# Optimization experiments

Measured on AMD Instinct MI355X. Metric: run time of the kernel, lower is better.

Reference implementation:

```python
import jax, jax.numpy as jnp
import numpy as np

TAU = 0.1
N, D = 8192, 128
NUM_CLASSES = 100


def setup_inputs() -> dict:
    key = jax.random.key(0)
    kx, ky = jax.random.split(key)
    x = jax.random.normal(kx, (N, D), dtype=jnp.float32)
    y = jax.random.randint(ky, (N,), 0, NUM_CLASSES, dtype=jnp.int64)
    return {"x": x, "y": y}


def reference(x, y):
    # cosine similarity matrix: S[i,j] = <x_i, x_j> / (||x_i|| ||x_j||)
    norms = jnp.linalg.norm(x, axis=-1, keepdims=True)  # [N,1]
    xn = x / norms
    sim = jnp.einsum('id,jd->ij', xn, xn)               # [N,N]
    e = jnp.exp(sim / TAU)                              # [N,N]
    same = (y[:, None] == y[None, :])                   # [N,N] bool (includes self, as in original)
    top = jnp.sum(jnp.where(same, e, 0.0), axis=1)      # [N]
    down = jnp.sum(e, axis=1)                           # [N]
    loss = jnp.mean(-jnp.log(top / down))
    return loss
```

## Files before the change

kernel.cpp:

```cpp
#include <hip/hip_runtime.h>
#include <hip/hip_bf16.h>
#include <stdint.h>

#define NROWS 8192
#define DDIM  128
#define NCHUNK 16
#define ROWS_PER_BLOCK 128
#define COLS_PER_BLOCK 512
#define GROUP_COLS 64
#define GROUP_BYTES (GROUP_COLS * DDIM)
#define NGROUPS (COLS_PER_BLOCK / GROUP_COLS)

typedef __attribute__((ext_vector_type(4))) float f32x4;
typedef long f8x8;

__device__ __forceinline__ void load_lds16(const void* g, void* l) {
    __builtin_amdgcn_global_load_lds(
        (const __attribute__((address_space(1))) void*)g,
        (__attribute__((address_space(3))) void*)l, 16, 0, 0);
}

#define SCALE 14.426950408889634f
#define E10   22026.465794806718f

__global__ __launch_bounds__(256) void normalize_kernel(
    const float* __restrict__ x, unsigned short* __restrict__ q16,
    float* __restrict__ dsq)
{
    int wave = threadIdx.x >> 6;
    int lane = threadIdx.x & 63;
    int row  = blockIdx.x * 4 + wave;
    const float2* xr = (const float2*)(x + (size_t)row * DDIM);
    float2 v = xr[lane];
    float ss = v.x * v.x + v.y * v.y;
    #pragma unroll
    for (int off = 1; off < 64; off <<= 1)
        ss += __shfl_xor(ss, off, 64);
    float rn = sqrtf(SCALE / ss);
    int pk = __builtin_amdgcn_cvt_pk_fp8_f32(v.x * rn, v.y * rn, 0, false);
    q16[(size_t)row * 64 + lane] = (unsigned short)(pk & 0xffff);
    float d0 = __builtin_amdgcn_cvt_f32_fp8(pk, 0);
    float d1 = __builtin_amdgcn_cvt_f32_fp8(pk, 1);
    float sq = d0 * d0 + d1 * d1;
    #pragma unroll
    for (int off = 1; off < 64; off <<= 1)
        sq += __shfl_xor(sq, off, 64);
    if (lane == 0) dsq[row] = sq;
}

__global__ __launch_bounds__(256, 4) void sim_kernel(
    const unsigned short* __restrict__ q16, const int* __restrict__ y,
    float* __restrict__ topp, float* __restrict__ downp)
{
    __shared__ char smem[2 * GROUP_BYTES];
    __shared__ int  yl[COLS_PER_BLOCK];

    const int bid  = blockIdx.x;
    const int iblk = bid >> 4;
    const int h    = bid & 15;
    const int tid  = threadIdx.x;
    const int lane = tid & 63;
    const int wave = tid >> 6;
    const int lrow = lane & 15;
    const int lhi  = lane >> 4;

    const char* qb = (const char*)q16;
    const int rbase = iblk * ROWS_PER_BLOCK + wave * 32;
    const int jbase = h * COLS_PER_BLOCK;

    yl[tid]       = y[jbase + tid];
    yl[tid + 256] = y[jbase + tid + 256];

    f8x8 afrag[2][4];
    #pragma unroll
    for (int t = 0; t < 2; ++t)
        #pragma unroll
        for (int ks = 0; ks < 4; ++ks)
            afrag[t][ks] = *(const f8x8*)(qb +
                (size_t)(rbase + t * 16 + lrow) * DDIM + ks * 32 + lhi * 8);

    int yrow[2][4];
    #pragma unroll
    for (int t = 0; t < 2; ++t)
        #pragma unroll
        for (int r = 0; r < 4; ++r)
            yrow[t][r] = y[rbase + t * 16 + lhi * 4 + r];

    float top[2][4]  = {{0.f,0.f,0.f,0.f},{0.f,0.f,0.f,0.f}};
    float down[2][4] = {{0.f,0.f,0.f,0.f},{0.f,0.f,0.f,0.f}};

    auto stage = [&](int buf, int g) {
        const int jstart = jbase + g * GROUP_COLS;
        #pragma unroll
        for (int p = 0; p < 2; ++p) {
            int phys = p * 4096 + tid * 16;
            int col  = phys >> 7;
            int L    = phys ^ ((col & 7) << 4);
            const char* src = qb + (size_t)(jstart + col) * DDIM + (L & 127);
            load_lds16(src, smem + buf * GROUP_BYTES + phys);
        }
    };

    stage(0, 0);
    __syncthreads();

    for (int g = 0; g < NGROUPS; ++g) {
        if (g + 1 < NGROUPS) stage((g + 1) & 1, g + 1);

        const char* lbuf = smem + (g & 1) * GROUP_BYTES;

        #pragma unroll
        for (int jt = 0; jt < GROUP_COLS / 16; ++jt) {
            const int cg = jt * 16 + lrow;
            const int ycol = yl[g * GROUP_COLS + cg];
            f8x8 bfrag[4];
            #pragma unroll
            for (int ks = 0; ks < 4; ++ks) {
                int off = cg * DDIM + ((ks * 32 + lhi * 8) ^ ((cg & 7) << 4));
                bfrag[ks] = *(const f8x8*)(lbuf + off);
            }
            #pragma unroll
            for (int t = 0; t < 2; ++t) {
                f32x4 acc = {0.f, 0.f, 0.f, 0.f};
                #pragma unroll
                for (int ks = 0; ks < 4; ++ks)
                    acc = __builtin_amdgcn_mfma_f32_16x16x32_fp8_fp8(
                        afrag[t][ks], bfrag[ks], acc, 0, 0, 0);
                #pragma unroll
                for (int r = 0; r < 4; ++r) {
                    float e = __builtin_amdgcn_exp2f(acc[r]);
                    down[t][r] += e;
                    top[t][r]  += (yrow[t][r] == ycol) ? e : 0.0f;
                }
            }
        }
        __syncthreads();
    }

    #pragma unroll
    for (int m = 1; m < 16; m <<= 1) {
        #pragma unroll
        for (int t = 0; t < 2; ++t)
            #pragma unroll
            for (int r = 0; r < 4; ++r) {
                top[t][r]  += __shfl_xor(top[t][r],  m, 64);
                down[t][r] += __shfl_xor(down[t][r], m, 64);
            }
    }

    if (lrow == 0) {
        #pragma unroll
        for (int t = 0; t < 2; ++t)
            #pragma unroll
            for (int r = 0; r < 4; ++r) {
                int row = rbase + t * 16 + lhi * 4 + r;
                topp [h * NROWS + row] = top[t][r];
                downp[h * NROWS + row] = down[t][r];
            }
    }
}

__global__ __launch_bounds__(64) void loss_partial_kernel(
    const float* __restrict__ topp, const float* __restrict__ downp,
    const float* __restrict__ dsq, float* __restrict__ partial)
{
    const int lane = threadIdx.x;
    const int r = blockIdx.x * 64 + lane;
    float t = 0.f, d = 0.f;
    #pragma unroll
    for (int hh = 0; hh < NCHUNK; ++hh) {
        t += topp [hh * NROWS + r];
        d += downp[hh * NROWS + r];
    }
    float e2d = __builtin_amdgcn_exp2f(dsq[r]);
    t = t - e2d + E10;
    d = d - e2d + E10;
    float s = __logf(d) - __logf(t);
    #pragma unroll
    for (int off = 1; off < 64; off <<= 1)
        s += __shfl_xor(s, off, 64);
    if (lane == 0) partial[blockIdx.x] = s;
}

__global__ __launch_bounds__(64) void loss_final_kernel(
    const float* __restrict__ partial, float* __restrict__ out)
{
    const int lane = threadIdx.x;
    float s = partial[lane] + partial[lane + 64];
    #pragma unroll
    for (int off = 1; off < 64; off <<= 1)
        s += __shfl_xor(s, off, 64);
    if (lane == 0) out[0] = s / (float)NROWS;
}

extern "C" void kernel_launch(void* const* d_in, const int* in_sizes, int n_in,
                              void* d_out, int out_size, void* d_ws, size_t ws_size,
                              hipStream_t stream)
{
    const float* x = (const float*)d_in[0];
    const int*   y = (const int*)d_in[1];
    float* out = (float*)d_out;

    char* ws = (char*)d_ws;
    unsigned short* q16 = (unsigned short*)ws;
    float* topp  = (float*)(ws + (size_t)NROWS * DDIM);
    float* downp = topp + NCHUNK * NROWS;
    float* dsq     = downp + NCHUNK * NROWS;
    float* partial = dsq + NROWS;

    normalize_kernel<<<NROWS / 4, 256, 0, stream>>>(x, q16, dsq);
    sim_kernel<<<64 * NCHUNK, 256, 0, stream>>>(q16, y, topp, downp);
    loss_partial_kernel<<<NROWS / 64, 64, 0, stream>>>(topp, downp, dsq, partial);
    loss_final_kernel<<<1, 64, 0, stream>>>(partial, out);
}
```

Measured before the change: 36.30 us.

## Retile sim kernel to 256x256 tiles with single-shot LDS panel load

The similarity kernel now gives each block 256 rows by 256 columns: each wave keeps 64 rows of A fragments in registers, and the whole 32KB column panel is loaded into LDS once up front. This replaces the 128x512 tiling and its double-buffered 64-column staging. Each B fragment read from LDS is now reused across four row tiles instead of two, and the per-group barriers go away. The cost is more registers per thread, which may reduce occupancy. There is also no overlap between the panel load and compute, and the number of column chunks the later reduction must sum doubles.

```diff
diff --git a/kernel.cpp b/kernel.cpp
--- a/kernel.cpp
+++ b/kernel.cpp
@@ -4,12 +4,10 @@
 
 #define NROWS 8192
 #define DDIM  128
-#define NCHUNK 16
-#define ROWS_PER_BLOCK 128
-#define COLS_PER_BLOCK 512
-#define GROUP_COLS 64
-#define GROUP_BYTES (GROUP_COLS * DDIM)
-#define NGROUPS (COLS_PER_BLOCK / GROUP_COLS)
+#define NCHUNK 32
+#define ROWS_PER_BLOCK 256
+#define COLS_PER_BLOCK 256
+#define PANEL_BYTES (COLS_PER_BLOCK * DDIM)
 
 typedef __attribute__((ext_vector_type(4))) float f32x4;
 typedef long f8x8;
@@ -52,12 +50,12 @@
     const unsigned short* __restrict__ q16, const int* __restrict__ y,
     float* __restrict__ topp, float* __restrict__ downp)
 {
-    __shared__ char smem[2 * GROUP_BYTES];
+    __shared__ char smem[PANEL_BYTES];
     __shared__ int  yl[COLS_PER_BLOCK];
 
     const int bid  = blockIdx.x;
-    const int iblk = bid >> 4;
-    const int h    = bid & 15;
+    const int iblk = bid >> 5;
+    const int h    = bid & 31;
     const int tid  = threadIdx.x;
     const int lane = tid & 63;
     const int wave = tid >> 6;
@@ -65,82 +63,70 @@
     const int lhi  = lane >> 4;
 
     const char* qb = (const char*)q16;
-    const int rbase = iblk * ROWS_PER_BLOCK + wave * 32;
+    const int rbase = iblk * ROWS_PER_BLOCK + wave * 64;
     const int jbase = h * COLS_PER_BLOCK;
 
-    yl[tid]       = y[jbase + tid];
-    yl[tid + 256] = y[jbase + tid + 256];
-
-    f8x8 afrag[2][4];
-    #pragma unroll
-    for (int t = 0; t < 2; ++t)
+    yl[tid] = y[jbase + tid];
+
+    #pragma unroll
+    for (int p = 0; p < 8; ++p) {
+        int phys = p * 4096 + tid * 16;
+        int col  = phys >> 7;
+        int L    = phys ^ ((col & 7) << 4);
+        const char* src = qb + (size_t)(jbase + col) * DDIM + (L & 127);
+        load_lds16(src, smem + phys);
+    }
+
+    f8x8 afrag[4][4];
+    #pragma unroll
+    for (int t = 0; t < 4; ++t)
         #pragma unroll
         for (int ks = 0; ks < 4; ++ks)
             afrag[t][ks] = *(const f8x8*)(qb +
                 (size_t)(rbase + t * 16 + lrow) * DDIM + ks * 32 + lhi * 8);
 
-    int yrow[2][4];
-    #pragma unroll
-    for (int t = 0; t < 2; ++t)
+    int yrow[4][4];
+    #pragma unroll
+    for (int t = 0; t < 4; ++t)
         #pragma unroll
         for (int r = 0; r < 4; ++r)
             yrow[t][r] = y[rbase + t * 16 + lhi * 4 + r];
 
-    float top[2][4]  = {{0.f,0.f,0.f,0.f},{0.f,0.f,0.f,0.f}};
-    float down[2][4] = {{0.f,0.f,0.f,0.f},{0.f,0.f,0.f,0.f}};
-
-    auto stage = [&](int buf, int g) {
-        const int jstart = jbase + g * GROUP_COLS;
-        #pragma unroll
-        for (int p = 0; p < 2; ++p) {
-            int phys = p * 4096 + tid * 16;
-            int col  = phys >> 7;
-            int L    = phys ^ ((col & 7) << 4);
-            const char* src = qb + (size_t)(jstart + col) * DDIM + (L & 127);
-            load_lds16(src, smem + buf * GROUP_BYTES + phys);
+    float top[4][4]  = {};
+    float down[4][4] = {};
+
+    __syncthreads();
+
+    #pragma unroll 2
+    for (int jt = 0; jt < COLS_PER_BLOCK / 16; ++jt) {
+        const int cg = jt * 16 + lrow;
+        const int ycol = yl[cg];
+        f8x8 bfrag[4];
+        #pragma unroll
+        for (int ks = 0; ks < 4; ++ks) {
+            int off = cg * DDIM + ((ks * 32 + lhi * 8) ^ ((cg & 7) << 4));
+            bfrag[ks] = *(const f8x8*)(smem + off);
         }
-    };
-
-    stage(0, 0);
-    __syncthreads();
-
-    for (int g = 0; g < NGROUPS; ++g) {
-        if (g + 1 < NGROUPS) stage((g + 1) & 1, g + 1);
-
-        const char* lbuf = smem + (g & 1) * GROUP_BYTES;
-
-        #pragma unroll
-        for (int jt = 0; jt < GROUP_COLS / 16; ++jt) {
-            const int cg = jt * 16 + lrow;
-            const int ycol = yl[g * GROUP_COLS + cg];
-            f8x8 bfrag[4];
-            #pragma unroll
-            for (int ks = 0; ks < 4; ++ks) {
-                int off = cg * DDIM + ((ks * 32 + lhi * 8) ^ ((cg & 7) << 4));
-                bfrag[ks] = *(const f8x8*)(lbuf + off);
-            }
-            #pragma unroll
-            for (int t = 0; t < 2; ++t) {
-                f32x4 acc = {0.f, 0.f, 0.f, 0.f};
-                #pragma unroll
-                for (int ks = 0; ks < 4; ++ks)
-                    acc = __builtin_amdgcn_mfma_f32_16x16x32_fp8_fp8(
-                        afrag[t][ks], bfrag[ks], acc, 0, 0, 0);
-                #pragma unroll
-                for (int r = 0; r < 4; ++r) {
-                    float e = __builtin_amdgcn_exp2f(acc[r]);
-                    down[t][r] += e;
-                    top[t][r]  += (yrow[t][r] == ycol) ? e : 0.0f;
-                }
+        #pragma unroll
+        for (int t = 0; t < 4; ++t) {
+            f32x4 acc = {0.f, 0.f, 0.f, 0.f};
+            #pragma unroll
+            for (int ks = 0; ks < 4; ++ks)
+                acc = __builtin_amdgcn_mfma_f32_16x16x32_fp8_fp8(
+                    afrag[t][ks], bfrag[ks], acc, 0, 0, 0);
+            #pragma unroll
+            for (int r = 0; r < 4; ++r) {
+                float e = __builtin_amdgcn_exp2f(acc[r]);
+                down[t][r] += e;
+                top[t][r]  += (yrow[t][r] == ycol) ? e : 0.0f;
             }
         }
-        __syncthreads();
     }
 
     #pragma unroll
     for (int m = 1; m < 16; m <<= 1) {
         #pragma unroll
-        for (int t = 0; t < 2; ++t)
+        for (int t = 0; t < 4; ++t)
             #pragma unroll
             for (int r = 0; r < 4; ++r) {
                 top[t][r]  += __shfl_xor(top[t][r],  m, 64);
@@ -150,7 +136,7 @@
 
     if (lrow == 0) {
         #pragma unroll
-        for (int t = 0; t < 2; ++t)
+        for (int t = 0; t < 4; ++t)
             #pragma unroll
             for (int r = 0; r < 4; ++r) {
                 int row = rbase + t * 16 + lhi * 4 + r;
@@ -209,7 +195,7 @@
     float* partial = dsq + NROWS;
 
     normalize_kernel<<<NROWS / 4, 256, 0, stream>>>(x, q16, dsq);
-    sim_kernel<<<64 * NCHUNK, 256, 0, stream>>>(q16, y, topp, downp);
+    sim_kernel<<<(NROWS / ROWS_PER_BLOCK) * NCHUNK, 256, 0, stream>>>(q16, y, topp, downp);
     loss_partial_kernel<<<NROWS / 64, 64, 0, stream>>>(topp, downp, dsq, partial);
     loss_final_kernel<<<1, 64, 0, stream>>>(partial, out);
 }
```

Measured after the change: 55.76 us. 1.54x slower.

## Exploit similarity symmetry by computing only upper-triangular tile pairs

Applied to the files above, without the earlier changes.

The similarity kernel now launches one block per unordered 128x128 tile pair (i<=j) and recovers the pair indices from a triangular index. Each off-diagonal tile adds its exp values to both row sums and column sums. Column partials are reduced across lanes and waves through LDS and written to the transposed slot, which roughly halves the MFMA and exp work. In exchange it adds column reduction, extra syncs and LDS, and the final reduction reads 64 partial chunks instead of 16, adding memory traffic.

```diff
diff --git a/kernel.cpp b/kernel.cpp
--- a/kernel.cpp
+++ b/kernel.cpp
@@ -4,12 +4,11 @@
 
 #define NROWS 8192
 #define DDIM  128
-#define NCHUNK 16
-#define ROWS_PER_BLOCK 128
-#define COLS_PER_BLOCK 512
-#define GROUP_COLS 64
-#define GROUP_BYTES (GROUP_COLS * DDIM)
-#define NGROUPS (COLS_PER_BLOCK / GROUP_COLS)
+#define NBLK  64
+#define NPAIR (NBLK * (NBLK + 1) / 2)
+#define BI 128
+#define BJ 128
+#define PANEL_BYTES (BJ * DDIM)
 
 typedef __attribute__((ext_vector_type(4))) float f32x4;
 typedef long f8x8;
@@ -52,12 +51,17 @@
     const unsigned short* __restrict__ q16, const int* __restrict__ y,
     float* __restrict__ topp, float* __restrict__ downp)
 {
-    __shared__ char smem[2 * GROUP_BYTES];
-    __shared__ int  yl[COLS_PER_BLOCK];
-
-    const int bid  = blockIdx.x;
-    const int iblk = bid >> 4;
-    const int h    = bid & 15;
+    __shared__ char  smem[PANEL_BYTES];
+    __shared__ int   yl[BJ];
+    __shared__ float scolD[4][BJ];
+    __shared__ float scolT[4][BJ];
+
+    int k = blockIdx.x;
+    int jb = (int)((sqrtf(8.0f * (float)k + 1.0f) - 1.0f) * 0.5f);
+    while ((jb + 1) * (jb + 2) / 2 <= k) ++jb;
+    while (jb * (jb + 1) / 2 > k) --jb;
+    int ib = k - jb * (jb + 1) / 2;
+
     const int tid  = threadIdx.x;
     const int lane = tid & 63;
     const int wave = tid >> 6;
@@ -65,11 +69,18 @@
     const int lhi  = lane >> 4;
 
     const char* qb = (const char*)q16;
-    const int rbase = iblk * ROWS_PER_BLOCK + wave * 32;
-    const int jbase = h * COLS_PER_BLOCK;
-
-    yl[tid]       = y[jbase + tid];
-    yl[tid + 256] = y[jbase + tid + 256];
+    const int rbase = ib * BI + wave * 32;
+    const int jbase = jb * BJ;
+
+    if (tid < BJ) yl[tid] = y[jbase + tid];
+
+    #pragma unroll
+    for (int p = 0; p < 4; ++p) {
+        int phys = p * 4096 + tid * 16;
+        int col  = phys >> 7;
+        int L    = phys ^ ((col & 7) << 4);
+        load_lds16(qb + (size_t)(jbase + col) * DDIM + (L & 127), smem + phys);
+    }
 
     f8x8 afrag[2][4];
     #pragma unroll
@@ -86,55 +97,40 @@
         for (int r = 0; r < 4; ++r)
             yrow[t][r] = y[rbase + t * 16 + lhi * 4 + r];
 
-    float top[2][4]  = {{0.f,0.f,0.f,0.f},{0.f,0.f,0.f,0.f}};
-    float down[2][4] = {{0.f,0.f,0.f,0.f},{0.f,0.f,0.f,0.f}};
-
-    auto stage = [&](int buf, int g) {
-        const int jstart = jbase + g * GROUP_COLS;
-        #pragma unroll
-        for (int p = 0; p < 2; ++p) {
-            int phys = p * 4096 + tid * 16;
-            int col  = phys >> 7;
-            int L    = phys ^ ((col & 7) << 4);
-            const char* src = qb + (size_t)(jstart + col) * DDIM + (L & 127);
-            load_lds16(src, smem + buf * GROUP_BYTES + phys);
+    __syncthreads();
+
+    float top[2][4]  = {};
+    float down[2][4] = {};
+    float colD[8] = {};
+    float colT[8] = {};
+
+    #pragma unroll
+    for (int jt = 0; jt < 8; ++jt) {
+        const int cg = jt * 16 + lrow;
+        const int ycol = yl[cg];
+        f8x8 bfrag[4];
+        #pragma unroll
+        for (int ks = 0; ks < 4; ++ks) {
+            int off = cg * DDIM + ((ks * 32 + lhi * 8) ^ ((cg & 7) << 4));
+            bfrag[ks] = *(const f8x8*)(smem + off);
         }
-    };
-
-    stage(0, 0);
-    __syncthreads();
-
-    for (int g = 0; g < NGROUPS; ++g) {
-        if (g + 1 < NGROUPS) stage((g + 1) & 1, g + 1);
-
-        const char* lbuf = smem + (g & 1) * GROUP_BYTES;
-
-        #pragma unroll
-        for (int jt = 0; jt < GROUP_COLS / 16; ++jt) {
-            const int cg = jt * 16 + lrow;
-            const int ycol = yl[g * GROUP_COLS + cg];
-            f8x8 bfrag[4];
-            #pragma unroll
-            for (int ks = 0; ks < 4; ++ks) {
-                int off = cg * DDIM + ((ks * 32 + lhi * 8) ^ ((cg & 7) << 4));
-                bfrag[ks] = *(const f8x8*)(lbuf + off);
-            }
-            #pragma unroll
-            for (int t = 0; t < 2; ++t) {
-                f32x4 acc = {0.f, 0.f, 0.f, 0.f};
-                #pragma unroll
-                for (int ks = 0; ks < 4; ++ks)
-                    acc = __builtin_amdgcn_mfma_f32_16x16x32_fp8_fp8(
-                        afrag[t][ks], bfrag[ks], acc, 0, 0, 0);
-                #pragma unroll
-                for (int r = 0; r < 4; ++r) {
-                    float e = __builtin_amdgcn_exp2f(acc[r]);
-                    down[t][r] += e;
-                    top[t][r]  += (yrow[t][r] == ycol) ? e : 0.0f;
-                }
+        #pragma unroll
+        for (int t = 0; t < 2; ++t) {
+            f32x4 acc = {0.f, 0.f, 0.f, 0.f};
+            #pragma unroll
+            for (int ks = 0; ks < 4; ++ks)
+                acc = __builtin_amdgcn_mfma_f32_16x16x32_fp8_fp8(
+                    afrag[t][ks], bfrag[ks], acc, 0, 0, 0);
+            #pragma unroll
+            for (int r = 0; r < 4; ++r) {
+                float e  = __builtin_amdgcn_exp2f(acc[r]);
+                float me = (yrow[t][r] == ycol) ? e : 0.0f;
+                down[t][r] += e;
+                top[t][r]  += me;
+                colD[jt] += e;
+                colT[jt] += me;
             }
         }
-        __syncthreads();
     }
 
     #pragma unroll
@@ -147,16 +143,37 @@
                 down[t][r] += __shfl_xor(down[t][r], m, 64);
             }
     }
-
     if (lrow == 0) {
         #pragma unroll
         for (int t = 0; t < 2; ++t)
             #pragma unroll
             for (int r = 0; r < 4; ++r) {
                 int row = rbase + t * 16 + lhi * 4 + r;
-                topp [h * NROWS + row] = top[t][r];
-                downp[h * NROWS + row] = down[t][r];
+                topp [jb * NROWS + row] = top[t][r];
+                downp[jb * NROWS + row] = down[t][r];
             }
+    }
+
+    #pragma unroll
+    for (int jt = 0; jt < 8; ++jt) {
+        colD[jt] += __shfl_xor(colD[jt], 16, 64);
+        colD[jt] += __shfl_xor(colD[jt], 32, 64);
+        colT[jt] += __shfl_xor(colT[jt], 16, 64);
+        colT[jt] += __shfl_xor(colT[jt], 32, 64);
+    }
+    if (lane < 16) {
+        #pragma unroll
+        for (int jt = 0; jt < 8; ++jt) {
+            scolD[wave][jt * 16 + lane] = colD[jt];
+            scolT[wave][jt * 16 + lane] = colT[jt];
+        }
+    }
+    __syncthreads();
+    if (ib != jb && tid < BJ) {
+        float cd = scolD[0][tid] + scolD[1][tid] + scolD[2][tid] + scolD[3][tid];
+        float ct = scolT[0][tid] + scolT[1][tid] + scolT[2][tid] + scolT[3][tid];
+        downp[ib * NROWS + jbase + tid] = cd;
+        topp [ib * NROWS + jbase + tid] = ct;
     }
 }
 
@@ -167,8 +184,8 @@
     const int lane = threadIdx.x;
     const int r = blockIdx.x * 64 + lane;
     float t = 0.f, d = 0.f;
-    #pragma unroll
-    for (int hh = 0; hh < NCHUNK; ++hh) {
+    #pragma unroll 8
+    for (int hh = 0; hh < NBLK; ++hh) {
         t += topp [hh * NROWS + r];
         d += downp[hh * NROWS + r];
     }
@@ -204,12 +221,12 @@
     char* ws = (char*)d_ws;
     unsigned short* q16 = (unsigned short*)ws;
     float* topp  = (float*)(ws + (size_t)NROWS * DDIM);
-    float* downp = topp + NCHUNK * NROWS;
-    float* dsq     = downp + NCHUNK * NROWS;
+    float* downp = topp + NBLK * NROWS;
+    float* dsq     = downp + NBLK * NROWS;
     float* partial = dsq + NROWS;
 
     normalize_kernel<<<NROWS / 4, 256, 0, stream>>>(x, q16, dsq);
-    sim_kernel<<<64 * NCHUNK, 256, 0, stream>>>(q16, y, topp, downp);
+    sim_kernel<<<NPAIR, 256, 0, stream>>>(q16, y, topp, downp);
     loss_partial_kernel<<<NROWS / 64, 64, 0, stream>>>(topp, downp, dsq, partial);
     loss_final_kernel<<<1, 64, 0, stream>>>(partial, out);
 }
```

Measured after the change: 62.04 us. 70.9% more time.
